# Optimization experiments

Measured on AMD Instinct MI355X. Metric: run time of the kernel, lower is better.

Reference implementation:

```python
import jax, jax.numpy as jnp
from jax import lax
import numpy as np

N, L, LQ, D, AF, K = 4096, 512, 32, 30, 10, 4  # n_sents, sent_len, q_len, embed_dim, extra feats, conv size


def setup_inputs() -> dict:
    key = jax.random.key(0)
    ks = jax.random.split(key, 10)
    fan_conv = 1.0 / np.sqrt(D * K)
    fan_lin = 1.0 / np.sqrt(AF + 3)
    return {
        "sents_embeds": jax.random.normal(ks[0], (N, L, D), jnp.float32),
        "question_embeds": jax.random.normal(ks[1], (LQ, D), jnp.float32),
        "sents_gaf": jax.random.normal(ks[2], (N, AF), jnp.float32),
        "sents_labels": jax.random.randint(ks[3], (N,), 0, 2),
        "conv1_w": jax.random.uniform(ks[4], (D, D, K), jnp.float32, -fan_conv, fan_conv),
        "conv1_b": jax.random.uniform(ks[5], (D,), jnp.float32, -fan_conv, fan_conv),
        "conv2_w": jax.random.uniform(ks[6], (D, D, K), jnp.float32, -fan_conv, fan_conv),
        "conv2_b": jax.random.uniform(ks[7], (D,), jnp.float32, -fan_conv, fan_conv),
        "lin_w": jax.random.uniform(ks[8], (2, AF + 3), jnp.float32, -fan_lin, fan_lin),
        "lin_b": jax.random.uniform(ks[9], (2,), jnp.float32, -fan_lin, fan_lin),
    }


def _conv1d(x, w, b):
    # x: [B, C, T], w: [O, I, K] (torch layout), padding = K-1 both sides (as torch padding=K-1)
    y = lax.conv_general_dilated(x, w, window_strides=(1,), padding=[(K - 1, K - 1)],
                                 dimension_numbers=("NCW", "OIW", "NCW"))
    return y + b[None, :, None]


def _window_pool(x):
    # avg_pool1d(kernel=K, stride=1) over last axis
    return lax.reduce_window(x, 0.0, lax.add, (1, 1, K), (1, 1, 1), "VALID") / K


def _gpool(x):
    # global average pool over last axis -> [B, C]
    return jnp.mean(x, axis=-1)


def _cos(a, b):
    # a: [N, D] or [D], b: [N, D] or [D] -> cosine similarity, broadcasting
    num = jnp.sum(a * b, axis=-1)
    den = jnp.linalg.norm(a, axis=-1) * jnp.linalg.norm(b, axis=-1)
    return num / den


def _forward(sents_embeds, question_embeds, sents_gaf, sents_labels,
             conv1_w, conv1_b, conv2_w, conv2_b, lin_w, lin_b):
    q = question_embeds.T[None]                # [1, D, LQ]
    s = jnp.transpose(sents_embeds, (0, 2, 1))  # [N, D, L]

    # question side (identical every loop iteration in the original)
    q_raw = _gpool(q)[0]                        # [D]
    q1c = _conv1d(q, conv1_w, conv1_b)          # [1, D, LQ+3]
    q1g = _gpool(q1c)[0]                        # [D]
    q1w = _window_pool(q1c)                     # [1, D, LQ]
    q2c = _conv1d(q1w, conv2_w, conv2_b)        # [1, D, LQ+3]
    q2g = _gpool(q2c)[0]                        # [D]

    # sentence side, batched over N
    s_raw = _gpool(s)                           # [N, D]
    s1c = _conv1d(s, conv1_w, conv1_b)          # [N, D, L+3]
    s1g = _gpool(s1c)                           # [N, D]
    s1w = _window_pool(s1c)                     # [N, D, L]
    s2c = _conv1d(s1w, conv2_w, conv2_b)        # [N, D, L+3]
    s2g = _gpool(s2c)                           # [N, D]

    # sim1: original overwrites quest_global_pool in the loop, so i=0 uses the raw
    # question pool and i>0 use the conv2-level question pool from the prior iter.
    sim1_raw = _cos(q_raw[None], s_raw)         # [N]
    sim1_q2 = _cos(q2g[None], s_raw)            # [N]
    sim1 = jnp.where(jnp.arange(s_raw.shape[0]) == 0, sim1_raw, sim1_q2)
    sim2 = _cos(q1g[None], s1g)                 # [N]
    sim3 = _cos(q2g[None], s2g)                 # [N]

    mlp_in = jnp.concatenate([sim1[:, None], sim2[:, None], sim3[:, None], sents_gaf], axis=-1)  # [N, 13]
    logits = mlp_in @ lin_w.T + lin_b           # [N, 2]
    logp = jax.nn.log_softmax(logits, axis=-1)
    cost = -jnp.mean(jnp.take_along_axis(logp, sents_labels[:, None], axis=-1)[:, 0])
    emit = jax.nn.softmax(logp, axis=-1)[:, 1]  # softmax applied to log_softmax, as in original
    return cost, emit


def reference(sents_embeds, question_embeds, sents_gaf, sents_labels,
              conv1_w, conv1_b, conv2_w, conv2_b, lin_w, lin_b):
    return _forward(sents_embeds, question_embeds, sents_gaf, sents_labels,
                    conv1_w, conv1_b, conv2_w, conv2_b, lin_w, lin_b)
```

## Files before the change

kernel.cpp:

```cpp
#include <hip/hip_runtime.h>
#include <math.h>

#define NS 4096
#define LL 512
#define LQS 32
#define DD 30
#define AFN 10
#define KW 4

enum {
  QRAW = 0,
  Q1G  = 30,
  Q2G  = 60,
  NRM  = 90,
  WS1  = 96,
  WS2  = 996,
  OA0  = 1896,
  OA1  = 2796,
  OA2  = 3696,
  OB0  = 4596,
  OB1  = 5496,
  OB2  = 6396,
  WTOT = 7296,
  LOSS = 7296
};

__global__ __launch_bounds__(256) void prep_kernel(
    const float* __restrict__ qe,
    const float* __restrict__ w1,
    const float* __restrict__ b1,
    const float* __restrict__ w2,
    const float* __restrict__ b2,
    float* __restrict__ ws,
    float* __restrict__ out)
{
    __shared__ float w1s[DD * DD * KW];
    __shared__ float w2s[DD * DD * KW];
    __shared__ float qT[DD][LQS];
    __shared__ float q1c[DD][LQS + 3];
    __shared__ float q1w[DD][LQS];
    __shared__ float q2c[DD][LQS + 3];
    __shared__ float qpool[3][DD];
    const int tid = threadIdx.x;

    for (int f = tid; f < DD * DD * KW; f += 256) {
        w1s[f] = w1[f];
        w2s[f] = w2[f];
    }
    for (int f = tid; f < LQS * DD; f += 256) {
        qT[f % DD][f / DD] = qe[f];
    }
    __syncthreads();

    for (int idx = tid; idx < DD * (LQS + 3); idx += 256) {
        int o = idx / (LQS + 3), t = idx % (LQS + 3);
        float acc = b1[o];
        for (int i = 0; i < DD; i++) {
            const float* w = w1s + (o * DD + i) * KW;
            #pragma unroll
            for (int k = 0; k < KW; k++) {
                int j = t + k - 3;
                if (j >= 0 && j < LQS) acc += qT[i][j] * w[k];
            }
        }
        q1c[o][t] = acc;
    }
    __syncthreads();

    for (int idx = tid; idx < DD * LQS; idx += 256) {
        int o = idx / LQS, t = idx % LQS;
        q1w[o][t] = 0.25f * (q1c[o][t] + q1c[o][t + 1] + q1c[o][t + 2] + q1c[o][t + 3]);
    }
    __syncthreads();

    for (int idx = tid; idx < DD * (LQS + 3); idx += 256) {
        int o = idx / (LQS + 3), t = idx % (LQS + 3);
        float acc = b2[o];
        for (int i = 0; i < DD; i++) {
            const float* w = w2s + (o * DD + i) * KW;
            #pragma unroll
            for (int k = 0; k < KW; k++) {
                int j = t + k - 3;
                if (j >= 0 && j < LQS) acc += q1w[i][j] * w[k];
            }
        }
        q2c[o][t] = acc;
    }
    __syncthreads();

    if (tid < DD) {
        float a = 0.f;
        for (int t = 0; t < LQS; t++) a += qT[tid][t];
        qpool[0][tid] = a * (1.0f / LQS);
        float g1 = 0.f;
        for (int t = 0; t < LQS + 3; t++) g1 += q1c[tid][t];
        qpool[1][tid] = g1 * (1.0f / (LQS + 3));
        float g2 = 0.f;
        for (int t = 0; t < LQS + 3; t++) g2 += q2c[tid][t];
        qpool[2][tid] = g2 * (1.0f / (LQS + 3));
        ws[QRAW + tid] = qpool[0][tid];
        ws[Q1G + tid]  = qpool[1][tid];
        ws[Q2G + tid]  = qpool[2][tid];
    }
    __syncthreads();
    if (tid < 3) {
        float s = 0.f;
        for (int i = 0; i < DD; i++) { float v = qpool[tid][i]; s += v * v; }
        ws[NRM + tid] = sqrtf(s);
    }
    if (tid >= 3 && tid < 6) ws[NRM + tid] = 0.f;
    if (tid == 0) out[0] = 0.0f;

    for (int idx = tid; idx < DD * DD; idx += 256) {
        int o = idx / DD, i = idx % DD;
        int tr = i * DD + o;
        const float* w = w1s + idx * KW;
        float a = w[0], b = w[1], c = w[2], d = w[3];
        ws[WS1 + tr] = a + b + c + d;
        ws[OA0 + tr] = 3.f * d + 2.f * c + b;
        ws[OA1 + tr] = 2.f * d + c;
        ws[OA2 + tr] = d;
        ws[OB0 + tr] = a;
        ws[OB1 + tr] = b + 2.f * a;
        ws[OB2 + tr] = c + 2.f * b + 3.f * a;
        const float* v = w2s + idx * KW;
        ws[WS2 + tr] = v[0] + v[1] + v[2] + v[3];
    }
}

__global__ __launch_bounds__(256) void stream_post_kernel(
    const float* __restrict__ se,
    const float* __restrict__ gaf,
    const int*   __restrict__ labels,
    const float* __restrict__ b1,
    const float* __restrict__ b2,
    const float* __restrict__ linw,
    const float* __restrict__ linb,
    const float* __restrict__ ws,
    float* __restrict__ lossbuf,
    float* __restrict__ out)
{
    const int n   = blockIdx.x;
    const int tid = threadIdx.x;
    const float* base = se + (size_t)n * (LL * DD);

    __shared__ float tabs[WTOT];
    __shared__ float partial[960];
    __shared__ float bnd[6][DD];

    {
        const float4* src = (const float4*)ws;
        float4* dst = (float4*)tabs;
        #pragma unroll
        for (int f = tid; f < WTOT / 4; f += 256) dst[f] = src[f];
    }
    if (tid < 240) {
        const float4* p = (const float4*)base + tid;
        float sx = 0.f, sy = 0.f, sz = 0.f, sw = 0.f;
        #pragma unroll
        for (int it = 0; it < 16; it++) {
            float4 v = p[it * 240];
            sx += v.x; sy += v.y; sz += v.z; sw += v.w;
        }
        partial[4 * tid + 0] = sx;
        partial[4 * tid + 1] = sy;
        partial[4 * tid + 2] = sz;
        partial[4 * tid + 3] = sw;
    }
    if (tid < 180) {
        int r = tid / DD, c = tid % DD;
        int j = (r < 3) ? r : (LL - 6 + r);
        bnd[r][c] = base[j * DD + c];
    }
    __syncthreads();

    if (tid < 64) {
        const int lane = tid;
        const bool act = (lane < DD);
        const int  ic  = act ? lane : 0;

        float S_i = 0.f;
        #pragma unroll
        for (int m = 0; m < 32; m++) S_i += partial[ic + DD * m];

        float e0r = bnd[0][ic], e1r = bnd[1][ic], e2r = bnd[2][ic];
        float e3r = bnd[3][ic], e4r = bnd[4][ic], e5r = bnd[5][ic];
        float bb1 = b1[ic], bb2 = b2[ic];

        float dotS = 0.f, edge = 0.f;
        #pragma unroll 6
        for (int ii = 0; ii < DD; ii++) {
            float s   = __shfl(S_i, ii, 64);
            float b0  = __shfl(e0r, ii, 64);
            float b1v = __shfl(e1r, ii, 64);
            float b2v = __shfl(e2r, ii, 64);
            float b3v = __shfl(e3r, ii, 64);
            float b4v = __shfl(e4r, ii, 64);
            float b5v = __shfl(e5r, ii, 64);
            const int t = ii * DD + ic;
            dotS += s * tabs[WS1 + t];
            edge += b0 * tabs[OA0 + t] + b1v * tabs[OA1 + t] + b2v * tabs[OA2 + t]
                  + b3v * tabs[OB0 + t] + b4v * tabs[OB1 + t] + b5v * tabs[OB2 + t];
        }
        float s1g = dotS * (1.0f / (LL + 3)) + bb1;
        float Tv  = dotS + (float)LL * bb1 - 0.25f * edge;

        float dot2 = 0.f;
        #pragma unroll 6
        for (int ii = 0; ii < DD; ii++) {
            float tv = __shfl(Tv, ii, 64);
            dot2 += tv * tabs[WS2 + ii * DD + ic];
        }
        float s2g = dot2 * (1.0f / (LL + 3)) + bb2;

        float qv = (n == 0) ? tabs[QRAW + ic] : tabs[Q2G + ic];
        float q1 = tabs[Q1G + ic];
        float q2 = tabs[Q2G + ic];
        float p0 = act ? qv * S_i : 0.f;
        float p1 = act ? S_i * S_i : 0.f;
        float p2 = act ? q1 * s1g : 0.f;
        float p3 = act ? s1g * s1g : 0.f;
        float p4 = act ? q2 * s2g : 0.f;
        float p5 = act ? s2g * s2g : 0.f;
        #pragma unroll
        for (int off = 32; off >= 1; off >>= 1) {
            p0 += __shfl_xor(p0, off, 64);
            p1 += __shfl_xor(p1, off, 64);
            p2 += __shfl_xor(p2, off, 64);
            p3 += __shfl_xor(p3, off, 64);
            p4 += __shfl_xor(p4, off, 64);
            p5 += __shfl_xor(p5, off, 64);
        }

        if (lane == 0) {
            float nq = (n == 0) ? tabs[NRM + 0] : tabs[NRM + 2];
            float sim1 = p0 / (nq * sqrtf(p1));
            float sim2 = p2 / (tabs[NRM + 1] * sqrtf(p3));
            float sim3 = p4 / (tabs[NRM + 2] * sqrtf(p5));

            float in[3 + AFN];
            in[0] = sim1; in[1] = sim2; in[2] = sim3;
            const float* g = gaf + (size_t)n * AFN;
            #pragma unroll
            for (int j = 0; j < AFN; j++) in[3 + j] = g[j];

            float l0 = linb[0], l1 = linb[1];
            #pragma unroll
            for (int j = 0; j < 3 + AFN; j++) {
                l0 += in[j] * linw[j];
                l1 += in[j] * linw[(3 + AFN) + j];
            }
            float m = fmaxf(l0, l1);
            float lse = m + logf(expf(l0 - m) + expf(l1 - m));
            float lp0 = l0 - lse, lp1 = l1 - lse;
            float mm = fmaxf(lp0, lp1);
            float ee0 = expf(lp0 - mm), ee1 = expf(lp1 - mm);
            out[1 + n] = ee1 / (ee0 + ee1);
            int lab = labels[n];
            lossbuf[n] = (lab == 0) ? lp0 : lp1;
        }
    }
}

__global__ __launch_bounds__(256) void loss_reduce_kernel(
    const float* __restrict__ lossbuf,
    float* __restrict__ out)
{
    __shared__ float wsum[4];
    const int tid = threadIdx.x;
    const float4* p = (const float4*)lossbuf;
    float s = 0.f;
    #pragma unroll
    for (int it = 0; it < 4; it++) {
        float4 v = p[tid + it * 256];
        s += v.x + v.y + v.z + v.w;
    }
    #pragma unroll
    for (int off = 32; off >= 1; off >>= 1) s += __shfl_xor(s, off, 64);
    if ((tid & 63) == 0) wsum[tid >> 6] = s;
    __syncthreads();
    if (tid == 0) out[0] = -(wsum[0] + wsum[1] + wsum[2] + wsum[3]) * (1.0f / NS);
}

extern "C" void kernel_launch(void* const* d_in, const int* in_sizes, int n_in,
                              void* d_out, int out_size, void* d_ws, size_t ws_size,
                              hipStream_t stream)
{
    (void)in_sizes; (void)n_in; (void)out_size; (void)ws_size;
    const float* se  = (const float*)d_in[0];
    const float* qe  = (const float*)d_in[1];
    const float* gaf = (const float*)d_in[2];
    const int*   lab = (const int*)d_in[3];
    const float* w1  = (const float*)d_in[4];
    const float* b1  = (const float*)d_in[5];
    const float* w2  = (const float*)d_in[6];
    const float* b2  = (const float*)d_in[7];
    const float* lw  = (const float*)d_in[8];
    const float* lb  = (const float*)d_in[9];
    float* out = (float*)d_out;
    float* ws  = (float*)d_ws;

    hipLaunchKernelGGL(prep_kernel, dim3(1), dim3(256), 0, stream,
                       qe, w1, b1, w2, b2, ws, out);
    hipLaunchKernelGGL(stream_post_kernel, dim3(NS), dim3(256), 0, stream,
                       se, gaf, lab, b1, b2, lw, lb, ws, ws + LOSS, out);
    hipLaunchKernelGGL(loss_reduce_kernel, dim3(1), dim3(256), 0, stream,
                       ws + LOSS, out);
}
```

Baseline: 418.8 us.

## Split streaming reduction across four blocks per sentence and separate post-processing kernel

Splits the fused per-sentence kernel into a streaming kernel, where each sentence's 512x30 embeddings are summed by four blocks writing partial sums and boundary rows to workspace, and a separate post kernel that handles four sentences per block with one wave each. This removes the 29 KB weight-table load into shared memory from every streaming block, which should raise occupancy and parallelism on the bandwidth-bound sum over 250 MB of input. The cost is an extra kernel launch and a small round-trip of partial sums through global memory.

```diff
diff --git a/kernel.cpp b/kernel.cpp
--- a/kernel.cpp
+++ b/kernel.cpp
@@ -7,6 +7,9 @@
 #define DD 30
 #define AFN 10
 #define KW 4
+#define QTR 4
+#define NBLKA (NS * QTR)
+#define QFLT (LL * DD / QTR)
 
 enum {
   QRAW = 0,
@@ -22,7 +25,9 @@
   OB1  = 5496,
   OB2  = 6396,
   WTOT = 7296,
-  LOSS = 7296
+  LOSS = 7296,
+  PBUF = LOSS + NS,
+  BNDB = PBUF + NBLKA * DD
 };
 
 __global__ __launch_bounds__(256) void prep_kernel(
@@ -128,8 +133,50 @@
     }
 }
 
-__global__ __launch_bounds__(256) void stream_post_kernel(
+__global__ __launch_bounds__(256) void stream_kernel(
     const float* __restrict__ se,
+    float* __restrict__ ws)
+{
+    const int blk = blockIdx.x;
+    const int n = blk >> 2, q = blk & 3;
+    const int tid = threadIdx.x;
+    const float* base = se + (size_t)n * (LL * DD);
+    const float* qb = base + q * QFLT;
+
+    __shared__ float partial[960];
+
+    if (tid < 240) {
+        const float4* p = (const float4*)qb + tid;
+        float sx = 0.f, sy = 0.f, sz = 0.f, sw = 0.f;
+        #pragma unroll
+        for (int it = 0; it < 4; it++) {
+            float4 v = p[it * 240];
+            sx += v.x; sy += v.y; sz += v.z; sw += v.w;
+        }
+        partial[4 * tid + 0] = sx;
+        partial[4 * tid + 1] = sy;
+        partial[4 * tid + 2] = sz;
+        partial[4 * tid + 3] = sw;
+    }
+    if (q == 0 && tid < 90) {
+        int r = tid / DD, c = tid % DD;
+        ws[BNDB + n * 180 + r * DD + c] = base[r * DD + c];
+    }
+    if (q == 3 && tid < 90) {
+        int r = tid / DD, c = tid % DD;
+        ws[BNDB + n * 180 + (3 + r) * DD + c] = base[(LL - 3 + r) * DD + c];
+    }
+    __syncthreads();
+
+    if (tid < DD) {
+        float S = 0.f;
+        #pragma unroll
+        for (int m = 0; m < 32; m++) S += partial[tid + DD * m];
+        ws[PBUF + blk * DD + tid] = S;
+    }
+}
+
+__global__ __launch_bounds__(256) void post_kernel(
     const float* __restrict__ gaf,
     const int*   __restrict__ labels,
     const float* __restrict__ b1,
@@ -140,125 +187,101 @@
     float* __restrict__ lossbuf,
     float* __restrict__ out)
 {
-    const int n   = blockIdx.x;
     const int tid = threadIdx.x;
-    const float* base = se + (size_t)n * (LL * DD);
-
     __shared__ float tabs[WTOT];
-    __shared__ float partial[960];
-    __shared__ float bnd[6][DD];
 
     {
         const float4* src = (const float4*)ws;
         float4* dst = (float4*)tabs;
+        for (int f = tid; f < WTOT / 4; f += 256) dst[f] = src[f];
+    }
+    __syncthreads();
+
+    const int w    = tid >> 6;
+    const int lane = tid & 63;
+    const int n    = blockIdx.x * 4 + w;
+    const bool act = (lane < DD);
+    const int  ic  = act ? lane : 0;
+
+    const float* pb = ws + PBUF + (size_t)(n * 4) * DD;
+    float S_i = pb[ic] + pb[DD + ic] + pb[2 * DD + ic] + pb[3 * DD + ic];
+
+    const float* bb = ws + BNDB + (size_t)n * 180;
+    float e0r = bb[0 * DD + ic], e1r = bb[1 * DD + ic], e2r = bb[2 * DD + ic];
+    float e3r = bb[3 * DD + ic], e4r = bb[4 * DD + ic], e5r = bb[5 * DD + ic];
+    float bb1 = b1[ic], bb2 = b2[ic];
+
+    float dotS = 0.f, edge = 0.f;
+    #pragma unroll 6
+    for (int ii = 0; ii < DD; ii++) {
+        float s   = __shfl(S_i, ii, 64);
+        float b0  = __shfl(e0r, ii, 64);
+        float b1v = __shfl(e1r, ii, 64);
+        float b2v = __shfl(e2r, ii, 64);
+        float b3v = __shfl(e3r, ii, 64);
+        float b4v = __shfl(e4r, ii, 64);
+        float b5v = __shfl(e5r, ii, 64);
+        const int t = ii * DD + ic;
+        dotS += s * tabs[WS1 + t];
+        edge += b0 * tabs[OA0 + t] + b1v * tabs[OA1 + t] + b2v * tabs[OA2 + t]
+              + b3v * tabs[OB0 + t] + b4v * tabs[OB1 + t] + b5v * tabs[OB2 + t];
+    }
+    float s1g = dotS * (1.0f / (LL + 3)) + bb1;
+    float Tv  = dotS + (float)LL * bb1 - 0.25f * edge;
+
+    float dot2 = 0.f;
+    #pragma unroll 6
+    for (int ii = 0; ii < DD; ii++) {
+        float tv = __shfl(Tv, ii, 64);
+        dot2 += tv * tabs[WS2 + ii * DD + ic];
+    }
+    float s2g = dot2 * (1.0f / (LL + 3)) + bb2;
+
+    float qv = (n == 0) ? tabs[QRAW + ic] : tabs[Q2G + ic];
+    float q1 = tabs[Q1G + ic];
+    float q2 = tabs[Q2G + ic];
+    float p0 = act ? qv * S_i : 0.f;
+    float p1 = act ? S_i * S_i : 0.f;
+    float p2 = act ? q1 * s1g : 0.f;
+    float p3 = act ? s1g * s1g : 0.f;
+    float p4 = act ? q2 * s2g : 0.f;
+    float p5 = act ? s2g * s2g : 0.f;
+    #pragma unroll
+    for (int off = 32; off >= 1; off >>= 1) {
+        p0 += __shfl_xor(p0, off, 64);
+        p1 += __shfl_xor(p1, off, 64);
+        p2 += __shfl_xor(p2, off, 64);
+        p3 += __shfl_xor(p3, off, 64);
+        p4 += __shfl_xor(p4, off, 64);
+        p5 += __shfl_xor(p5, off, 64);
+    }
+
+    if (lane == 0) {
+        float nq = (n == 0) ? tabs[NRM + 0] : tabs[NRM + 2];
+        float sim1 = p0 / (nq * sqrtf(p1));
+        float sim2 = p2 / (tabs[NRM + 1] * sqrtf(p3));
+        float sim3 = p4 / (tabs[NRM + 2] * sqrtf(p5));
+
+        float in[3 + AFN];
+        in[0] = sim1; in[1] = sim2; in[2] = sim3;
+        const float* g = gaf + (size_t)n * AFN;
         #pragma unroll
-        for (int f = tid; f < WTOT / 4; f += 256) dst[f] = src[f];
-    }
-    if (tid < 240) {
-        const float4* p = (const float4*)base + tid;
-        float sx = 0.f, sy = 0.f, sz = 0.f, sw = 0.f;
+        for (int j = 0; j < AFN; j++) in[3 + j] = g[j];
+
+        float l0 = linb[0], l1 = linb[1];
         #pragma unroll
-        for (int it = 0; it < 16; it++) {
-            float4 v = p[it * 240];
-            sx += v.x; sy += v.y; sz += v.z; sw += v.w;
+        for (int j = 0; j < 3 + AFN; j++) {
+            l0 += in[j] * linw[j];
+            l1 += in[j] * linw[(3 + AFN) + j];
         }
-        partial[4 * tid + 0] = sx;
-        partial[4 * tid + 1] = sy;
-        partial[4 * tid + 2] = sz;
-        partial[4 * tid + 3] = sw;
-    }
-    if (tid < 180) {
-        int r = tid / DD, c = tid % DD;
-        int j = (r < 3) ? r : (LL - 6 + r);
-        bnd[r][c] = base[j * DD + c];
-    }
-    __syncthreads();
-
-    if (tid < 64) {
-        const int lane = tid;
-        const bool act = (lane < DD);
-        const int  ic  = act ? lane : 0;
-
-        float S_i = 0.f;
-        #pragma unroll
-        for (int m = 0; m < 32; m++) S_i += partial[ic + DD * m];
-
-        float e0r = bnd[0][ic], e1r = bnd[1][ic], e2r = bnd[2][ic];
-        float e3r = bnd[3][ic], e4r = bnd[4][ic], e5r = bnd[5][ic];
-        float bb1 = b1[ic], bb2 = b2[ic];
-
-        float dotS = 0.f, edge = 0.f;
-        #pragma unroll 6
-        for (int ii = 0; ii < DD; ii++) {
-            float s   = __shfl(S_i, ii, 64);
-            float b0  = __shfl(e0r, ii, 64);
-            float b1v = __shfl(e1r, ii, 64);
-            float b2v = __shfl(e2r, ii, 64);
-            float b3v = __shfl(e3r, ii, 64);
-            float b4v = __shfl(e4r, ii, 64);
-            float b5v = __shfl(e5r, ii, 64);
-            const int t = ii * DD + ic;
-            dotS += s * tabs[WS1 + t];
-            edge += b0 * tabs[OA0 + t] + b1v * tabs[OA1 + t] + b2v * tabs[OA2 + t]
-                  + b3v * tabs[OB0 + t] + b4v * tabs[OB1 + t] + b5v * tabs[OB2 + t];
-        }
-        float s1g = dotS * (1.0f / (LL + 3)) + bb1;
-        float Tv  = dotS + (float)LL * bb1 - 0.25f * edge;
-
-        float dot2 = 0.f;
-        #pragma unroll 6
-        for (int ii = 0; ii < DD; ii++) {
-            float tv = __shfl(Tv, ii, 64);
-            dot2 += tv * tabs[WS2 + ii * DD + ic];
-        }
-        float s2g = dot2 * (1.0f / (LL + 3)) + bb2;
-
-        float qv = (n == 0) ? tabs[QRAW + ic] : tabs[Q2G + ic];
-        float q1 = tabs[Q1G + ic];
-        float q2 = tabs[Q2G + ic];
-        float p0 = act ? qv * S_i : 0.f;
-        float p1 = act ? S_i * S_i : 0.f;
-        float p2 = act ? q1 * s1g : 0.f;
-        float p3 = act ? s1g * s1g : 0.f;
-        float p4 = act ? q2 * s2g : 0.f;
-        float p5 = act ? s2g * s2g : 0.f;
-        #pragma unroll
-        for (int off = 32; off >= 1; off >>= 1) {
-            p0 += __shfl_xor(p0, off, 64);
-            p1 += __shfl_xor(p1, off, 64);
-            p2 += __shfl_xor(p2, off, 64);
-            p3 += __shfl_xor(p3, off, 64);
-            p4 += __shfl_xor(p4, off, 64);
-            p5 += __shfl_xor(p5, off, 64);
-        }
-
-        if (lane == 0) {
-            float nq = (n == 0) ? tabs[NRM + 0] : tabs[NRM + 2];
-            float sim1 = p0 / (nq * sqrtf(p1));
-            float sim2 = p2 / (tabs[NRM + 1] * sqrtf(p3));
-            float sim3 = p4 / (tabs[NRM + 2] * sqrtf(p5));
-
-            float in[3 + AFN];
-            in[0] = sim1; in[1] = sim2; in[2] = sim3;
-            const float* g = gaf + (size_t)n * AFN;
-            #pragma unroll
-            for (int j = 0; j < AFN; j++) in[3 + j] = g[j];
-
-            float l0 = linb[0], l1 = linb[1];
-            #pragma unroll
-            for (int j = 0; j < 3 + AFN; j++) {
-                l0 += in[j] * linw[j];
-                l1 += in[j] * linw[(3 + AFN) + j];
-            }
-            float m = fmaxf(l0, l1);
-            float lse = m + logf(expf(l0 - m) + expf(l1 - m));
-            float lp0 = l0 - lse, lp1 = l1 - lse;
-            float mm = fmaxf(lp0, lp1);
-            float ee0 = expf(lp0 - mm), ee1 = expf(lp1 - mm);
-            out[1 + n] = ee1 / (ee0 + ee1);
-            int lab = labels[n];
-            lossbuf[n] = (lab == 0) ? lp0 : lp1;
-        }
+        float m = fmaxf(l0, l1);
+        float lse = m + logf(expf(l0 - m) + expf(l1 - m));
+        float lp0 = l0 - lse, lp1 = l1 - lse;
+        float mm = fmaxf(lp0, lp1);
+        float ee0 = expf(lp0 - mm), ee1 = expf(lp1 - mm);
+        out[1 + n] = ee1 / (ee0 + ee1);
+        int lab = labels[n];
+        lossbuf[n] = (lab == 0) ? lp0 : lp1;
     }
 }
 
@@ -302,8 +325,10 @@
 
     hipLaunchKernelGGL(prep_kernel, dim3(1), dim3(256), 0, stream,
                        qe, w1, b1, w2, b2, ws, out);
-    hipLaunchKernelGGL(stream_post_kernel, dim3(NS), dim3(256), 0, stream,
-                       se, gaf, lab, b1, b2, lw, lb, ws, ws + LOSS, out);
+    hipLaunchKernelGGL(stream_kernel, dim3(NBLKA), dim3(256), 0, stream,
+                       se, ws);
+    hipLaunchKernelGGL(post_kernel, dim3(NS / 4), dim3(256), 0, stream,
+                       gaf, lab, b1, b2, lw, lb, ws, ws + LOSS, out);
     hipLaunchKernelGGL(loss_reduce_kernel, dim3(1), dim3(256), 0, stream,
                        ws + LOSS, out);
 }
```

Result: slower. 432.2 us (+3.2%).
